# Performance work log

Hardware: AMD Instinct MI355X
Metric: run time of the kernel (lower is better)

Reference implementation:

```python
import jax, jax.numpy as jnp
import numpy as np

EPS = 1e-5

def _bn(x, gamma, beta):
    # BatchNorm with track_running_stats=False: batch stats over all dims but last
    axes = tuple(range(x.ndim - 1))
    mu = jnp.mean(x, axis=axes)
    var = jnp.var(x, axis=axes)  # biased, as torch uses for normalization
    return (x - mu) * jax.lax.rsqrt(var + EPS) * gamma + beta

def setup_inputs() -> dict:
    B, N, D = 8, 200, 128
    key = jax.random.key(0)
    ks = jax.random.split(key, 14)
    s = 1.0 / np.sqrt(D)
    def w(k):
        return jax.random.uniform(k, (D, D), jnp.float32, -s, s)
    def b(k):
        return jax.random.uniform(k, (D,), jnp.float32, -s, s)
    return {
        'h': jax.random.normal(ks[0], (B, N, D), jnp.float32),
        'e': jax.random.normal(ks[1], (B, N, N, D), jnp.float32),
        'Uw': w(ks[2]), 'Ub': b(ks[3]),
        'Vw': w(ks[4]), 'Vb': b(ks[5]),
        'Aw': w(ks[6]), 'Ab': b(ks[7]),
        'Bw': w(ks[8]), 'Bb': b(ks[9]),
        'Cw': w(ks[10]), 'Cb': b(ks[11]),
        'gamma_h': jnp.ones((D,), jnp.float32), 'beta_h': jnp.zeros((D,), jnp.float32),
        'gamma_e': jnp.ones((D,), jnp.float32), 'beta_e': jnp.zeros((D,), jnp.float32),
    }

def reference(h, e, Uw, Ub, Vw, Vb, Aw, Ab, Bw, Bb, Cw, Cb,
              gamma_h, beta_h, gamma_e, beta_e):
    h_in, e_in = h, e
    Uh = h @ Uw.T + Ub                      # [B,N,D]
    Vh = h @ Vw.T + Vb                      # [B,N,D]
    Ah = h @ Aw.T + Ab
    Bh = h @ Bw.T + Bb
    Ce = e @ Cw.T + Cb                      # [B,N,N,D]
    # e_new[b,i,j,d] = Ah[b,j,d] + Bh[b,i,d] + Ce[b,i,j,d]
    e_new = Ah[:, None, :, :] + Bh[:, :, None, :] + Ce
    gates = jax.nn.sigmoid(e_new)           # [B,N,N,D]
    # sum aggregation over source nodes j with Vh broadcast over i
    agg = jnp.sum(gates * Vh[:, None, :, :], axis=2)  # [B,N,D]
    h_new = Uh + agg
    h_out = h_in + jax.nn.relu(_bn(h_new, gamma_h, beta_h))
    e_out = e_in + jax.nn.relu(_bn(e_new, gamma_e, beta_e))
    return (h_out, e_out)
```

## Files before the change

### kernel.cpp

```cpp
#include <hip/hip_runtime.h>
#include <hip/hip_bf16.h>


#define B_ 8
#define N_ 200
#define D_ 128
#define BN_ (B_*N_)
#define HN_ (BN_*D_)

typedef __attribute__((ext_vector_type(8))) short short8v;
typedef __attribute__((ext_vector_type(4))) short short4v;
typedef __attribute__((ext_vector_type(4))) float float4v;
typedef __attribute__((ext_vector_type(4))) unsigned int uint4v;

__device__ __forceinline__ unsigned short f2b(float f) {
  unsigned u = __float_as_uint(f);
  u += 0x7FFFu + ((u >> 16) & 1u);
  return (unsigned short)(u >> 16);
}

__global__ __launch_bounds__(256) void prelin_kernel(
    const float* __restrict__ h,
    const float* __restrict__ Uw, const float* __restrict__ Ub,
    const float* __restrict__ Vw, const float* __restrict__ Vb,
    const float* __restrict__ Aw, const float* __restrict__ Ab,
    const float* __restrict__ Bw, const float* __restrict__ Bb,
    const float* __restrict__ Cw,
    float* __restrict__ Uh, float* __restrict__ Vh,
    float* __restrict__ Ah, float* __restrict__ Bh,
    unsigned short* __restrict__ Cwbf) {
  const int tid = threadIdx.x;
  if (blockIdx.x >= 100) {
    int g = (blockIdx.x - 100) * 1024 + tid * 4;
    float4v v = *(const float4v*)(Cw + g);
    short4v s;
    s.x = (short)f2b(v.x); s.y = (short)f2b(v.y);
    s.z = (short)f2b(v.z); s.w = (short)f2b(v.w);
    *(short4v*)(Cwbf + g) = s;
    return;
  }
  const int r0 = blockIdx.x * 16;
  __shared__ float hs[16][128];
  for (int k = 0; k < 2; k++) {
    int g = k * 256 + tid;
    int row = g >> 5, col4 = g & 31;
    *(float4v*)&hs[row][col4 * 4] =
        *(const float4v*)(h + (size_t)(r0 + row) * D_ + col4 * 4);
  }
  __syncthreads();
  const int c0 = tid, c1 = tid + 256;
  const float* w0 = (c0 < 128) ? (Uw + c0 * 128) : (Vw + (c0 - 128) * 128);
  const float  b0 = (c0 < 128) ? Ub[c0] : Vb[c0 - 128];
  const float* w1 = (c1 < 384) ? (Aw + (c1 - 256) * 128) : (Bw + (c1 - 384) * 128);
  const float  b1 = (c1 < 384) ? Ab[c1 - 256] : Bb[c1 - 384];
  float acc0[16], acc1[16];
#pragma unroll
  for (int r = 0; r < 16; r++) { acc0[r] = 0.f; acc1[r] = 0.f; }
  for (int k = 0; k < 128; k += 4) {
    float4v w0v = *(const float4v*)(w0 + k);
    float4v w1v = *(const float4v*)(w1 + k);
#pragma unroll
    for (int r = 0; r < 16; r++) {
      float4v hv = *(const float4v*)&hs[r][k];
      acc0[r] = fmaf(hv.x, w0v.x, fmaf(hv.y, w0v.y, fmaf(hv.z, w0v.z, fmaf(hv.w, w0v.w, acc0[r]))));
      acc1[r] = fmaf(hv.x, w1v.x, fmaf(hv.y, w1v.y, fmaf(hv.z, w1v.z, fmaf(hv.w, w1v.w, acc1[r]))));
    }
  }
  float* dst0 = (c0 < 128) ? Uh : Vh; const int cc0 = c0 & 127;
  float* dst1 = (c1 < 384) ? Ah : Bh; const int cc1 = (c1 - 256) & 127;
#pragma unroll
  for (int r = 0; r < 16; r++) {
    dst0[(size_t)(r0 + r) * D_ + cc0] = acc0[r] + b0;
    dst1[(size_t)(r0 + r) * D_ + cc1] = acc1[r] + b1;
  }
}

template <int MODE>
__global__ __launch_bounds__(256, 2) void gemm_pass(
    const float* __restrict__ e, const unsigned short* __restrict__ Cwbf,
    const float* __restrict__ Cb, const float* __restrict__ Ah,
    const float* __restrict__ Bh, const float* __restrict__ Vh,
    float* __restrict__ agg, float* __restrict__ psum, float* __restrict__ psumsq,
    const float* __restrict__ scale_e, const float* __restrict__ shift_e,
    float* __restrict__ e_out) {
  const int tid = threadIdx.x;
  const int blk = blockIdx.x;
  const int b = blk / N_;
  const int lane = tid & 63, wz = tid >> 6;
  const int c = lane & 15, q = lane >> 4;

  __shared__ __align__(16) unsigned short Bs[128 * 136];
  __shared__ float base_s[128];
  __shared__ float ss_s[256];

  const uint4v* bsrc = (const uint4v*)Cwbf;
#pragma unroll
  for (int k2 = 0; k2 < 8; k2++) {
    int g = k2 * 256 + tid;
    int row = g >> 4, col = (g & 15) * 8;
    *(uint4v*)&Bs[row * 136 + col] = bsrc[g];
  }
  if (tid < 128) {
    base_s[tid] = Cb[tid] + Bh[(size_t)blk * D_ + tid];
    if (MODE == 1) { ss_s[tid] = scale_e[tid]; ss_s[128 + tid] = shift_e[tid]; }
  }
  __syncthreads();

  const float* erow = e + (size_t)blk * N_ * D_;
  const float* AhB = Ah + (size_t)b * N_ * D_;
  const float* VhB = (MODE == 0) ? (Vh + (size_t)b * N_ * D_) : nullptr;

  float aggv[8], sumv[8], sqv[8];
  if (MODE == 0) {
#pragma unroll
    for (int t = 0; t < 8; t++) { aggv[t] = 0.f; sumv[t] = 0.f; sqv[t] = 0.f; }
  }

  float4v ef[8];
  {
    const int j = wz * 16 + c;
    const float* p = erow + (size_t)j * D_ + q * 8;
    const bool ok = (j < N_);
#pragma unroll
    for (int l = 0; l < 4; l++) {
      ef[2 * l]     = ok ? *(const float4v*)(p + l * 32)     : (float4v){0.f,0.f,0.f,0.f};
      ef[2 * l + 1] = ok ? *(const float4v*)(p + l * 32 + 4) : (float4v){0.f,0.f,0.f,0.f};
    }
  }

#pragma unroll
  for (int jt = 0; jt < 4; jt++) {
    const int j0 = jt * 64;
    short8v av[4];
#pragma unroll
    for (int l = 0; l < 4; l++) {
      float4v v0 = ef[2 * l], v1 = ef[2 * l + 1];
      short8v s;
      s[0] = (short)f2b(v0.x); s[1] = (short)f2b(v0.y);
      s[2] = (short)f2b(v0.z); s[3] = (short)f2b(v0.w);
      s[4] = (short)f2b(v1.x); s[5] = (short)f2b(v1.y);
      s[6] = (short)f2b(v1.z); s[7] = (short)f2b(v1.w);
      av[l] = s;
    }
    if (jt < 3) {
      const int j = (jt + 1) * 64 + wz * 16 + c;
      const float* p = erow + (size_t)j * D_ + q * 8;
      const bool ok = (j < N_);
#pragma unroll
      for (int l = 0; l < 4; l++) {
        ef[2 * l]     = ok ? *(const float4v*)(p + l * 32)     : (float4v){0.f,0.f,0.f,0.f};
        ef[2 * l + 1] = ok ? *(const float4v*)(p + l * 32 + 4) : (float4v){0.f,0.f,0.f,0.f};
      }
    }

    float4v acc[8];
#pragma unroll
    for (int t = 0; t < 8; t++) acc[t] = (float4v){0.f, 0.f, 0.f, 0.f};
#pragma unroll
    for (int t = 0; t < 8; t++) {
      const unsigned short* brow = &Bs[(t * 16 + c) * 136 + q * 8];
#pragma unroll
      for (int l = 0; l < 4; l++) {
        short8v cw = *(const short8v*)(brow + l * 32);
        if (MODE == 0)
          acc[t] = __builtin_amdgcn_mfma_f32_16x16x32_bf16(av[l], cw, acc[t], 0, 0, 0);
        else
          acc[t] = __builtin_amdgcn_mfma_f32_16x16x32_bf16(cw, av[l], acc[t], 0, 0, 0);
      }
    }

    if (MODE == 0) {
#pragma unroll
      for (int t = 0; t < 8; t++) {
        const int n = t * 16 + c;
        const float bse = base_s[n];
#pragma unroll
        for (int r = 0; r < 4; r++) {
          const int j = j0 + wz * 16 + q * 4 + r;
          if (j < N_) {
            float x = acc[t][r] + bse + AhB[(size_t)j * D_ + n];
            float g = __builtin_amdgcn_rcpf(1.0f + __expf(-x));
            aggv[t] += g * VhB[(size_t)j * D_ + n];
            sumv[t] += x;
            sqv[t] += x * x;
          }
        }
      }
    } else {
      const int j = j0 + wz * 16 + c;
      if (j < N_) {
        const size_t rowoff = (size_t)blk * N_ * D_ + (size_t)j * D_;
#pragma unroll
        for (int t = 0; t < 8; t++) {
          const int n4 = t * 16 + q * 4;
          float4v ah = *(const float4v*)(AhB + (size_t)j * D_ + n4);
          float4v bs4 = *(const float4v*)&base_s[n4];
          float4v sc4 = *(const float4v*)&ss_s[n4];
          float4v sh4 = *(const float4v*)&ss_s[128 + n4];
          float4v ein = *(const float4v*)(e + rowoff + n4);
          float4v o;
#pragma unroll
          for (int r = 0; r < 4; r++) {
            float x = acc[t][r] + bs4[r] + ah[r];
            float y = fmaxf(x * sc4[r] + sh4[r], 0.f);
            o[r] = ein[r] + y;
          }
          *(float4v*)(e_out + rowoff + n4) = o;
        }
      }
    }
  }

  if (MODE == 0) {
    __syncthreads();
    float* red = (float*)Bs;
#pragma unroll
    for (int t = 0; t < 8; t++) {
      float a = aggv[t], s = sumv[t], sq2 = sqv[t];
      a += __shfl_xor(a, 16); a += __shfl_xor(a, 32);
      s += __shfl_xor(s, 16); s += __shfl_xor(s, 32);
      sq2 += __shfl_xor(sq2, 16); sq2 += __shfl_xor(sq2, 32);
      if (q == 0) {
        red[(0 * 4 + wz) * 128 + t * 16 + c] = a;
        red[(1 * 4 + wz) * 128 + t * 16 + c] = s;
        red[(2 * 4 + wz) * 128 + t * 16 + c] = sq2;
      }
    }
    __syncthreads();
    if (tid < 128) {
      float a = 0.f, s = 0.f, sq2 = 0.f;
#pragma unroll
      for (int w = 0; w < 4; w++) {
        a += red[(0 * 4 + w) * 128 + tid];
        s += red[(1 * 4 + w) * 128 + tid];
        sq2 += red[(2 * 4 + w) * 128 + tid];
      }
      agg[(size_t)blk * D_ + tid] = a;
      psum[(size_t)blk * D_ + tid] = s;
      psumsq[(size_t)blk * D_ + tid] = sq2;
    }
  }
}

__global__ __launch_bounds__(256) void stats_part(
    const float* __restrict__ psum, const float* __restrict__ psumsq,
    const float* __restrict__ Uh, const float* __restrict__ agg,
    float* __restrict__ partial) {
  const int t = threadIdx.x, blk = blockIdx.x;
  const int cg = t & 31, rs = t >> 5;
  float4v ps = {0,0,0,0}, pq = {0,0,0,0}, hs = {0,0,0,0}, hq = {0,0,0,0};
#pragma unroll
  for (int p = 0; p < 2; p++) {
    const int row = blk * 16 + p * 8 + rs;
    const size_t off = (size_t)row * D_ + cg * 4;
    float4v a = *(const float4v*)(psum + off);
    float4v bq = *(const float4v*)(psumsq + off);
    float4v u = *(const float4v*)(Uh + off);
    float4v g = *(const float4v*)(agg + off);
    ps += a; pq += bq;
    float4v hv = u + g;
    hs += hv; hq += hv * hv;
  }
  __shared__ float4v red[4][8][32];
  red[0][rs][cg] = ps; red[1][rs][cg] = pq; red[2][rs][cg] = hs; red[3][rs][cg] = hq;
  __syncthreads();
  if (t < 128) {
    const int s = t >> 5, g = t & 31;
    float4v acc = red[s][0][g];
#pragma unroll
    for (int r = 1; r < 8; r++) acc += red[s][r][g];
    *(float4v*)(partial + (size_t)blk * 512 + s * 128 + g * 4) = acc;
  }
}

__global__ __launch_bounds__(128) void stats_final(
    const float* __restrict__ partial,
    const float* __restrict__ gamma_h, const float* __restrict__ beta_h,
    const float* __restrict__ gamma_e, const float* __restrict__ beta_e,
    float* __restrict__ scale_e, float* __restrict__ shift_e,
    float* __restrict__ scale_h, float* __restrict__ shift_h) {
  const int n = threadIdx.x;
  float s = 0.f, sq = 0.f, hs = 0.f, hq = 0.f;
  for (int p = 0; p < 100; p++) {
    const float* base = partial + (size_t)p * 512;
    s += base[n]; sq += base[128 + n]; hs += base[256 + n]; hq += base[384 + n];
  }
  const float Me = 8.f * 200.f * 200.f;
  float mean = s / Me;
  float var = sq / Me - mean * mean;
  float sce = gamma_e[n] * rsqrtf(var + 1e-5f);
  scale_e[n] = sce; shift_e[n] = beta_e[n] - mean * sce;
  const float Mh = (float)BN_;
  float mh = hs / Mh;
  float vh = hq / Mh - mh * mh;
  float sch = gamma_h[n] * rsqrtf(vh + 1e-5f);
  scale_h[n] = sch; shift_h[n] = beta_h[n] - mh * sch;
}

__global__ __launch_bounds__(256) void hpath_kernel(
    const float* __restrict__ h, const float* __restrict__ Uh,
    const float* __restrict__ agg, const float* __restrict__ scale_h,
    const float* __restrict__ shift_h, float* __restrict__ h_out) {
  const int idx = blockIdx.x * 256 + threadIdx.x;
  float4v u = ((const float4v*)Uh)[idx];
  float4v a = ((const float4v*)agg)[idx];
  float4v hv = ((const float4v*)h)[idx];
  float4v sc = ((const float4v*)scale_h)[idx & 31];
  float4v sh = ((const float4v*)shift_h)[idx & 31];
  float4v o;
#pragma unroll
  for (int l = 0; l < 4; l++) {
    float y = fmaxf((u[l] + a[l]) * sc[l] + sh[l], 0.f);
    o[l] = hv[l] + y;
  }
  ((float4v*)h_out)[idx] = o;
}

extern "C" void kernel_launch(void* const* d_in, const int* in_sizes, int n_in,
                              void* d_out, int out_size, void* d_ws, size_t ws_size,
                              hipStream_t stream) {
  const float* h  = (const float*)d_in[0];
  const float* e  = (const float*)d_in[1];
  const float* Uw = (const float*)d_in[2];  const float* Ub = (const float*)d_in[3];
  const float* Vw = (const float*)d_in[4];  const float* Vb = (const float*)d_in[5];
  const float* Aw = (const float*)d_in[6];  const float* Ab = (const float*)d_in[7];
  const float* Bw = (const float*)d_in[8];  const float* Bb = (const float*)d_in[9];
  const float* Cw = (const float*)d_in[10]; const float* Cb = (const float*)d_in[11];
  const float* gamma_h = (const float*)d_in[12]; const float* beta_h = (const float*)d_in[13];
  const float* gamma_e = (const float*)d_in[14]; const float* beta_e = (const float*)d_in[15];

  float* ws = (float*)d_ws;
  float* Uh = ws + 0;
  float* Vh = ws + (size_t)HN_;
  float* Ah = ws + (size_t)HN_ * 2;
  float* Bh = ws + (size_t)HN_ * 3;
  float* agg = ws + (size_t)HN_ * 4;
  float* psum = ws + (size_t)HN_ * 5;
  float* psumsq = ws + (size_t)HN_ * 6;
  float* scale_e = ws + (size_t)HN_ * 7;
  float* shift_e = scale_e + 128;
  float* scale_h = scale_e + 256;
  float* shift_h = scale_e + 384;
  unsigned short* Cwbf = (unsigned short*)(scale_e + 512);
  float* partial = scale_e + 512 + 8192;

  float* h_out = (float*)d_out;
  float* e_out = (float*)d_out + HN_;

  prelin_kernel<<<116, 256, 0, stream>>>(h, Uw, Ub, Vw, Vb, Aw, Ab, Bw, Bb, Cw,
                                         Uh, Vh, Ah, Bh, Cwbf);
  gemm_pass<0><<<BN_, 256, 0, stream>>>(e, Cwbf, Cb, Ah, Bh, Vh,
                                        agg, psum, psumsq,
                                        nullptr, nullptr, nullptr);
  stats_part<<<100, 256, 0, stream>>>(psum, psumsq, Uh, agg, partial);
  stats_final<<<1, 128, 0, stream>>>(partial, gamma_h, beta_h, gamma_e, beta_e,
                                     scale_e, shift_e, scale_h, shift_h);
  hpath_kernel<<<200, 256, 0, stream>>>(h, Uh, agg, scale_h, shift_h, h_out);
  gemm_pass<1><<<BN_, 256, 0, stream>>>(e, Cwbf, Cb, Ah, Bh, nullptr,
                                        nullptr, nullptr, nullptr,
                                        scale_e, shift_e, e_out);
}
```

Before: 484.7 us.

## Split gemm blocks per 64-row tile, pre-swizzle Cw into MFMA fragment layout

Result: slower. 495.1 us (+2.2%).

```diff
diff --git a/kernel.cpp b/kernel.cpp
--- a/kernel.cpp
+++ b/kernel.cpp
@@ -28,15 +28,21 @@
     const float* __restrict__ Cw,
     float* __restrict__ Uh, float* __restrict__ Vh,
     float* __restrict__ Ah, float* __restrict__ Bh,
-    unsigned short* __restrict__ Cwbf) {
+    unsigned short* __restrict__ Cwf) {
   const int tid = threadIdx.x;
   if (blockIdx.x >= 100) {
-    int g = (blockIdx.x - 100) * 1024 + tid * 4;
-    float4v v = *(const float4v*)(Cw + g);
-    short4v s;
-    s.x = (short)f2b(v.x); s.y = (short)f2b(v.y);
-    s.z = (short)f2b(v.z); s.w = (short)f2b(v.w);
-    *(short4v*)(Cwbf + g) = s;
+    const int slot = (blockIdx.x - 100) * 256 + tid;
+    const int fr = slot >> 6, ln = slot & 63;
+    const int t = fr >> 2, l = fr & 3, cc = ln & 15, qq = ln >> 4;
+    const float* src = Cw + (t * 16 + cc) * 128 + l * 32 + qq * 8;
+    float4v v0 = *(const float4v*)src;
+    float4v v1 = *(const float4v*)(src + 4);
+    short8v s;
+    s[0] = (short)f2b(v0.x); s[1] = (short)f2b(v0.y);
+    s[2] = (short)f2b(v0.z); s[3] = (short)f2b(v0.w);
+    s[4] = (short)f2b(v1.x); s[5] = (short)f2b(v1.y);
+    s[6] = (short)f2b(v1.z); s[7] = (short)f2b(v1.w);
+    *(short8v*)(Cwf + (size_t)slot * 8) = s;
     return;
   }
   const int r0 = blockIdx.x * 16;
@@ -76,8 +82,8 @@
 }
 
 template <int MODE>
-__global__ __launch_bounds__(256, 2) void gemm_pass(
-    const float* __restrict__ e, const unsigned short* __restrict__ Cwbf,
+__global__ __launch_bounds__(256, 4) void gemm_pass(
+    const float* __restrict__ e, const unsigned short* __restrict__ Cwf,
     const float* __restrict__ Cb, const float* __restrict__ Ah,
     const float* __restrict__ Bh, const float* __restrict__ Vh,
     float* __restrict__ agg, float* __restrict__ psum, float* __restrict__ psumsq,
@@ -85,159 +91,114 @@
     float* __restrict__ e_out) {
   const int tid = threadIdx.x;
   const int blk = blockIdx.x;
-  const int b = blk / N_;
+  const int bi = blk >> 2, jt = blk & 3;
+  const int b = bi / N_;
   const int lane = tid & 63, wz = tid >> 6;
   const int c = lane & 15, q = lane >> 4;
-
-  __shared__ __align__(16) unsigned short Bs[128 * 136];
+  const int j0 = jt * 64;
+
+  __shared__ __align__(16) unsigned short Bs[16384];
   __shared__ float base_s[128];
   __shared__ float ss_s[256];
 
-  const uint4v* bsrc = (const uint4v*)Cwbf;
-#pragma unroll
-  for (int k2 = 0; k2 < 8; k2++) {
-    int g = k2 * 256 + tid;
-    int row = g >> 4, col = (g & 15) * 8;
-    *(uint4v*)&Bs[row * 136 + col] = bsrc[g];
+  const int jrow = j0 + wz * 16 + c;
+  const bool rok = (jrow < N_);
+  const float* ep = e + ((size_t)bi * N_ + jrow) * D_ + q * 8;
+  float4v ef[8];
+#pragma unroll
+  for (int l = 0; l < 4; l++) {
+    ef[2 * l]     = rok ? *(const float4v*)(ep + l * 32)     : (float4v){0.f,0.f,0.f,0.f};
+    ef[2 * l + 1] = rok ? *(const float4v*)(ep + l * 32 + 4) : (float4v){0.f,0.f,0.f,0.f};
+  }
+
+  {
+    const uint4v* bsrc = (const uint4v*)Cwf;
+    uint4v* bdst = (uint4v*)Bs;
+#pragma unroll
+    for (int k2 = 0; k2 < 8; k2++) bdst[k2 * 256 + tid] = bsrc[k2 * 256 + tid];
   }
   if (tid < 128) {
-    base_s[tid] = Cb[tid] + Bh[(size_t)blk * D_ + tid];
+    base_s[tid] = Cb[tid] + Bh[(size_t)bi * D_ + tid];
     if (MODE == 1) { ss_s[tid] = scale_e[tid]; ss_s[128 + tid] = shift_e[tid]; }
   }
+
+  short8v av[4];
+#pragma unroll
+  for (int l = 0; l < 4; l++) {
+    float4v v0 = ef[2 * l], v1 = ef[2 * l + 1];
+    short8v s;
+    s[0] = (short)f2b(v0.x); s[1] = (short)f2b(v0.y);
+    s[2] = (short)f2b(v0.z); s[3] = (short)f2b(v0.w);
+    s[4] = (short)f2b(v1.x); s[5] = (short)f2b(v1.y);
+    s[6] = (short)f2b(v1.z); s[7] = (short)f2b(v1.w);
+    av[l] = s;
+  }
   __syncthreads();
 
-  const float* erow = e + (size_t)blk * N_ * D_;
-  const float* AhB = Ah + (size_t)b * N_ * D_;
-  const float* VhB = (MODE == 0) ? (Vh + (size_t)b * N_ * D_) : nullptr;
-
-  float aggv[8], sumv[8], sqv[8];
+  float4v acc[8];
+#pragma unroll
+  for (int t = 0; t < 8; t++) acc[t] = (float4v){0.f, 0.f, 0.f, 0.f};
+#pragma unroll
+  for (int l = 0; l < 4; l++) {
+#pragma unroll
+    for (int t = 0; t < 8; t++) {
+      short8v cw = *(const short8v*)&Bs[(((t * 4 + l) * 64) + lane) * 8];
+      if (MODE == 0)
+        acc[t] = __builtin_amdgcn_mfma_f32_16x16x32_bf16(av[l], cw, acc[t], 0, 0, 0);
+      else
+        acc[t] = __builtin_amdgcn_mfma_f32_16x16x32_bf16(cw, av[l], acc[t], 0, 0, 0);
+    }
+  }
+
   if (MODE == 0) {
-#pragma unroll
-    for (int t = 0; t < 8; t++) { aggv[t] = 0.f; sumv[t] = 0.f; sqv[t] = 0.f; }
-  }
-
-  float4v ef[8];
-  {
-    const int j = wz * 16 + c;
-    const float* p = erow + (size_t)j * D_ + q * 8;
-    const bool ok = (j < N_);
-#pragma unroll
-    for (int l = 0; l < 4; l++) {
-      ef[2 * l]     = ok ? *(const float4v*)(p + l * 32)     : (float4v){0.f,0.f,0.f,0.f};
-      ef[2 * l + 1] = ok ? *(const float4v*)(p + l * 32 + 4) : (float4v){0.f,0.f,0.f,0.f};
-    }
-  }
-
-#pragma unroll
-  for (int jt = 0; jt < 4; jt++) {
-    const int j0 = jt * 64;
-    short8v av[4];
-#pragma unroll
-    for (int l = 0; l < 4; l++) {
-      float4v v0 = ef[2 * l], v1 = ef[2 * l + 1];
-      short8v s;
-      s[0] = (short)f2b(v0.x); s[1] = (short)f2b(v0.y);
-      s[2] = (short)f2b(v0.z); s[3] = (short)f2b(v0.w);
-      s[4] = (short)f2b(v1.x); s[5] = (short)f2b(v1.y);
-      s[6] = (short)f2b(v1.z); s[7] = (short)f2b(v1.w);
-      av[l] = s;
-    }
-    if (jt < 3) {
-      const int j = (jt + 1) * 64 + wz * 16 + c;
-      const float* p = erow + (size_t)j * D_ + q * 8;
-      const bool ok = (j < N_);
-#pragma unroll
-      for (int l = 0; l < 4; l++) {
-        ef[2 * l]     = ok ? *(const float4v*)(p + l * 32)     : (float4v){0.f,0.f,0.f,0.f};
-        ef[2 * l + 1] = ok ? *(const float4v*)(p + l * 32 + 4) : (float4v){0.f,0.f,0.f,0.f};
+    const float* AhB = Ah + (size_t)b * N_ * D_;
+    const float* VhB = Vh + (size_t)b * N_ * D_;
+#pragma unroll
+    for (int t = 0; t < 8; t++) {
+      const int n = t * 16 + c;
+      const float bse = base_s[n];
+      float at = 0.f, st = 0.f, qt = 0.f;
+#pragma unroll
+      for (int r = 0; r < 4; r++) {
+        const int j = j0 + wz * 16 + q * 4 + r;
+        if (j < N_) {
+          float x = acc[t][r] + bse + AhB[(size_t)j * D_ + n];
+          float g = __builtin_amdgcn_rcpf(1.0f + __expf(-x));
+          at += g * VhB[(size_t)j * D_ + n];
+          st += x; qt += x * x;
+        }
+      }
+      at += __shfl_xor(at, 16); at += __shfl_xor(at, 32);
+      st += __shfl_xor(st, 16); st += __shfl_xor(st, 32);
+      qt += __shfl_xor(qt, 16); qt += __shfl_xor(qt, 32);
+      if (lane < 16) {
+        atomicAdd(&agg[(size_t)bi * D_ + n], at);
+        atomicAdd(&psum[(size_t)bi * D_ + n], st);
+        atomicAdd(&psumsq[(size_t)bi * D_ + n], qt);
       }
     }
-
-    float4v acc[8];
-#pragma unroll
-    for (int t = 0; t < 8; t++) acc[t] = (float4v){0.f, 0.f, 0.f, 0.f};
-#pragma unroll
-    for (int t = 0; t < 8; t++) {
-      const unsigned short* brow = &Bs[(t * 16 + c) * 136 + q * 8];
-#pragma unroll
-      for (int l = 0; l < 4; l++) {
-        short8v cw = *(const short8v*)(brow + l * 32);
-        if (MODE == 0)
-          acc[t] = __builtin_amdgcn_mfma_f32_16x16x32_bf16(av[l], cw, acc[t], 0, 0, 0);
-        else
-          acc[t] = __builtin_amdgcn_mfma_f32_16x16x32_bf16(cw, av[l], acc[t], 0, 0, 0);
+  } else {
+    const int j = j0 + wz * 16 + c;
+    if (j < N_) {
+      const float* AhB = Ah + (size_t)b * N_ * D_;
+      const size_t rowoff = ((size_t)bi * N_ + j) * D_;
+#pragma unroll
+      for (int t = 0; t < 8; t++) {
+        const int n4 = t * 16 + q * 4;
+        float4v ah = *(const float4v*)(AhB + (size_t)j * D_ + n4);
+        float4v bs4 = *(const float4v*)&base_s[n4];
+        float4v sc4 = *(const float4v*)&ss_s[n4];
+        float4v sh4 = *(const float4v*)&ss_s[128 + n4];
+        float4v ein = *(const float4v*)(e + rowoff + n4);
+        float4v o;
+#pragma unroll
+        for (int r = 0; r < 4; r++) {
+          float x = acc[t][r] + bs4[r] + ah[r];
+          float y = fmaxf(x * sc4[r] + sh4[r], 0.f);
+          o[r] = ein[r] + y;
+        }
+        *(float4v*)(e_out + rowoff + n4) = o;
       }
-    }
-
-    if (MODE == 0) {
-#pragma unroll
-      for (int t = 0; t < 8; t++) {
-        const int n = t * 16 + c;
-        const float bse = base_s[n];
-#pragma unroll
-        for (int r = 0; r < 4; r++) {
-          const int j = j0 + wz * 16 + q * 4 + r;
-          if (j < N_) {
-            float x = acc[t][r] + bse + AhB[(size_t)j * D_ + n];
-            float g = __builtin_amdgcn_rcpf(1.0f + __expf(-x));
-            aggv[t] += g * VhB[(size_t)j * D_ + n];
-            sumv[t] += x;
-            sqv[t] += x * x;
-          }
-        }
-      }
-    } else {
-      const int j = j0 + wz * 16 + c;
-      if (j < N_) {
-        const size_t rowoff = (size_t)blk * N_ * D_ + (size_t)j * D_;
-#pragma unroll
-        for (int t = 0; t < 8; t++) {
-          const int n4 = t * 16 + q * 4;
-          float4v ah = *(const float4v*)(AhB + (size_t)j * D_ + n4);
-          float4v bs4 = *(const float4v*)&base_s[n4];
-          float4v sc4 = *(const float4v*)&ss_s[n4];
-          float4v sh4 = *(const float4v*)&ss_s[128 + n4];
-          float4v ein = *(const float4v*)(e + rowoff + n4);
-          float4v o;
-#pragma unroll
-          for (int r = 0; r < 4; r++) {
-            float x = acc[t][r] + bs4[r] + ah[r];
-            float y = fmaxf(x * sc4[r] + sh4[r], 0.f);
-            o[r] = ein[r] + y;
-          }
-          *(float4v*)(e_out + rowoff + n4) = o;
-        }
-      }
-    }
-  }
-
-  if (MODE == 0) {
-    __syncthreads();
-    float* red = (float*)Bs;
-#pragma unroll
-    for (int t = 0; t < 8; t++) {
-      float a = aggv[t], s = sumv[t], sq2 = sqv[t];
-      a += __shfl_xor(a, 16); a += __shfl_xor(a, 32);
-      s += __shfl_xor(s, 16); s += __shfl_xor(s, 32);
-      sq2 += __shfl_xor(sq2, 16); sq2 += __shfl_xor(sq2, 32);
-      if (q == 0) {
-        red[(0 * 4 + wz) * 128 + t * 16 + c] = a;
-        red[(1 * 4 + wz) * 128 + t * 16 + c] = s;
-        red[(2 * 4 + wz) * 128 + t * 16 + c] = sq2;
-      }
-    }
-    __syncthreads();
-    if (tid < 128) {
-      float a = 0.f, s = 0.f, sq2 = 0.f;
-#pragma unroll
-      for (int w = 0; w < 4; w++) {
-        a += red[(0 * 4 + w) * 128 + tid];
-        s += red[(1 * 4 + w) * 128 + tid];
-        sq2 += red[(2 * 4 + w) * 128 + tid];
-      }
-      agg[(size_t)blk * D_ + tid] = a;
-      psum[(size_t)blk * D_ + tid] = s;
-      psumsq[(size_t)blk * D_ + tid] = sq2;
     }
   }
 }
@@ -341,22 +302,23 @@
   float* shift_e = scale_e + 128;
   float* scale_h = scale_e + 256;
   float* shift_h = scale_e + 384;
-  unsigned short* Cwbf = (unsigned short*)(scale_e + 512);
+  unsigned short* Cwf = (unsigned short*)(scale_e + 512);
   float* partial = scale_e + 512 + 8192;
 
   float* h_out = (float*)d_out;
   float* e_out = (float*)d_out + HN_;
 
-  prelin_kernel<<<116, 256, 0, stream>>>(h, Uw, Ub, Vw, Vb, Aw, Ab, Bw, Bb, Cw,
-                                         Uh, Vh, Ah, Bh, Cwbf);
-  gemm_pass<0><<<BN_, 256, 0, stream>>>(e, Cwbf, Cb, Ah, Bh, Vh,
-                                        agg, psum, psumsq,
-                                        nullptr, nullptr, nullptr);
+  prelin_kernel<<<108, 256, 0, stream>>>(h, Uw, Ub, Vw, Vb, Aw, Ab, Bw, Bb, Cw,
+                                         Uh, Vh, Ah, Bh, Cwf);
+  hipMemsetAsync(agg, 0, (size_t)3 * HN_ * sizeof(float), stream);
+  gemm_pass<0><<<BN_ * 4, 256, 0, stream>>>(e, Cwf, Cb, Ah, Bh, Vh,
+                                            agg, psum, psumsq,
+                                            nullptr, nullptr, nullptr);
   stats_part<<<100, 256, 0, stream>>>(psum, psumsq, Uh, agg, partial);
   stats_final<<<1, 128, 0, stream>>>(partial, gamma_h, beta_h, gamma_e, beta_e,
                                      scale_e, shift_e, scale_h, shift_h);
   hpath_kernel<<<200, 256, 0, stream>>>(h, Uh, agg, scale_h, shift_h, h_out);
-  gemm_pass<1><<<BN_, 256, 0, stream>>>(e, Cwbf, Cb, Ah, Bh, nullptr,
-                                        nullptr, nullptr, nullptr,
-                                        scale_e, shift_e, e_out);
-}
+  gemm_pass<1><<<BN_ * 4, 256, 0, stream>>>(e, Cwf, Cb, Ah, Bh, nullptr,
+                                            nullptr, nullptr, nullptr,
+                                            scale_e, shift_e, e_out);
+}
```
